# Optimization experiments

Measured on AMD Instinct MI355X. Metric: run time of the kernel, lower is better.

Reference implementation:

```python
import jax, jax.numpy as jnp
import numpy as np

B, S, H = 2, 1024, 2048
E, K, F = 64, 8, 768
CAP = 512


def setup_inputs() -> dict:
    key = jax.random.key(0)
    k1, k2, k3, k4, k5 = jax.random.split(key, 5)
    scale_h = 1.0 / np.sqrt(H)
    scale_f = 1.0 / np.sqrt(F)
    return {
        "hidden_states": jax.random.normal(k1, (B, S, H), jnp.float32),
        "router_w": jax.random.normal(k2, (E, H), jnp.float32) * scale_h,   # MoEGate.weight [E, H]
        "w_gate": jax.random.normal(k3, (E, H, F), jnp.float32) * scale_h,
        "w_up": jax.random.normal(k4, (E, H, F), jnp.float32) * scale_h,
        "w_down": jax.random.normal(k5, (E, F, H), jnp.float32) * scale_f,
    }


def reference(hidden_states, router_w, w_gate, w_up, w_down):
    b, s, h = hidden_states.shape
    T = b * s
    xf = hidden_states.reshape(T, h)

    # --- MoEGate: softmax over expert logits, then top-k, then renormalize ---
    logits = xf @ router_w.T                                   # [T, E]
    scores = jax.nn.softmax(logits.astype(jnp.float32), axis=-1)
    topk_w, topk_idx = jax.lax.top_k(scores, K)                # [T, K]
    topk_w = topk_w / (topk_w.sum(axis=-1, keepdims=True) + 1e-20)

    # --- dispatch: scatter each (token, k) slot into a per-expert capacity buffer ---
    slot_expert = topk_idx.reshape(-1)                         # [T*K]
    slot_token = jnp.repeat(jnp.arange(T), K)                  # [T*K]
    onehot = jax.nn.one_hot(slot_expert, E, dtype=jnp.int32)   # [T*K, E]
    pos = (jnp.cumsum(onehot, axis=0) * onehot).sum(-1) - 1    # position within expert
    valid = pos < CAP
    dest = jnp.where(valid, slot_expert * CAP + pos, E * CAP)  # overflow -> dummy row

    buf = jnp.zeros((E * CAP + 1, h), xf.dtype).at[dest].set(xf[slot_token])
    xb = buf[: E * CAP].reshape(E, CAP, h)                     # [E, CAP, H]

    # --- grouped GEMM experts: SwiGLU MLP per expert ---
    gate = jnp.einsum("ech,ehf->ecf", xb, w_gate)
    up = jnp.einsum("ech,ehf->ecf", xb, w_up)
    hmid = jax.nn.silu(gate) * up                              # [E, CAP, F]
    yb = jnp.einsum("ecf,efh->ech", hmid, w_down).reshape(E * CAP, h)
    yb = jnp.concatenate([yb, jnp.zeros((1, h), yb.dtype)], axis=0)

    # --- combine: gather expert outputs back, weight, scatter-add per token ---
    slot_out = yb[dest] * topk_w.reshape(-1)[:, None].astype(yb.dtype)
    out = jnp.zeros((T, h), yb.dtype).at[slot_token].add(slot_out)
    return out.reshape(b, s, h)
```

## Files before the change

### kernel.cpp

```cpp
#include <hip/hip_runtime.h>
#include <math.h>

#define T_TOK 2048
#define HD    2048
#define NEXP  64
#define KTOP  8
#define FD    768
#define CAPE  512

typedef float  f32x4 __attribute__((ext_vector_type(4)));
typedef __bf16 bf16x8 __attribute__((ext_vector_type(8)));

__device__ __forceinline__ unsigned short f2bf(float f) {
  union { float f; unsigned u; } v; v.f = f;
  unsigned r = v.u + 0x7fffu + ((v.u >> 16) & 1u);
  return (unsigned short)(r >> 16);
}

__device__ __forceinline__ void load_lds16(const void* g, void* l) {
  __builtin_amdgcn_global_load_lds(
      (const __attribute__((address_space(1))) unsigned int*)g,
      (__attribute__((address_space(3))) unsigned int*)l, 16, 0, 0);
}

__global__ __launch_bounds__(256) void router_kernel(
    const float* __restrict__ x, const float* __restrict__ rw,
    int* __restrict__ cnt, int* __restrict__ tok_list, float* __restrict__ w_list)
{
  const int t = threadIdx.x;
  const int tb = blockIdx.x * 4;
  __shared__ float xs[4][HD];
  __shared__ float lg[4][NEXP];

  const float4* xsrc = (const float4*)(x + (size_t)tb * HD);
  float4* xdst = (float4*)&xs[0][0];
  for (int i = t; i < 4 * HD / 4; i += 256) xdst[i] = xsrc[i];
  __syncthreads();

  {
    const int e = t >> 2, q = t & 3;
    const float* wrow = rw + (size_t)e * HD;
    float a0 = 0.f, a1 = 0.f, a2 = 0.f, a3 = 0.f;
    for (int i = 0; i < HD / 16; ++i) {
      int h = (i * 4 + q) * 4;
      float4 wv = *(const float4*)(wrow + h);
      float4 x0 = *(const float4*)&xs[0][h];
      float4 x1 = *(const float4*)&xs[1][h];
      float4 x2 = *(const float4*)&xs[2][h];
      float4 x3 = *(const float4*)&xs[3][h];
      a0 += wv.x*x0.x + wv.y*x0.y + wv.z*x0.z + wv.w*x0.w;
      a1 += wv.x*x1.x + wv.y*x1.y + wv.z*x1.z + wv.w*x1.w;
      a2 += wv.x*x2.x + wv.y*x2.y + wv.z*x2.z + wv.w*x2.w;
      a3 += wv.x*x3.x + wv.y*x3.y + wv.z*x3.z + wv.w*x3.w;
    }
    a0 += __shfl_xor(a0, 1); a0 += __shfl_xor(a0, 2);
    a1 += __shfl_xor(a1, 1); a1 += __shfl_xor(a1, 2);
    a2 += __shfl_xor(a2, 1); a2 += __shfl_xor(a2, 2);
    a3 += __shfl_xor(a3, 1); a3 += __shfl_xor(a3, 2);
    if (q == 0) { lg[0][e] = a0; lg[1][e] = a1; lg[2][e] = a2; lg[3][e] = a3; }
  }
  __syncthreads();

  const int wid = t >> 6, lane = t & 63;
  float v = lg[wid][lane];
  float mx = v;
  for (int o = 32; o; o >>= 1) mx = fmaxf(mx, __shfl_xor(mx, o));
  float p = expf(v - mx);
  float s = p;
  for (int o = 32; o; o >>= 1) s += __shfl_xor(s, o);
  float prob = p / s;

  float r = prob;
  float wk[KTOP]; int ik[KTOP]; float wsum = 0.f;
  #pragma unroll
  for (int k = 0; k < KTOP; ++k) {
    float bv = r; int bl = lane;
    for (int o = 32; o; o >>= 1) {
      float ov = __shfl_xor(bv, o); int ol = __shfl_xor(bl, o);
      if (ov > bv || (ov == bv && ol < bl)) { bv = ov; bl = ol; }
    }
    wk[k] = bv; ik[k] = bl; wsum += bv;
    if (lane == bl) r = -1.f;
  }
  if (lane == 0) {
    float inv = 1.f / (wsum + 1e-20f);
    int token = tb + wid;
    #pragma unroll
    for (int k = 0; k < KTOP; ++k) {
      int ex = ik[k];
      int pos = atomicAdd(&cnt[ex], 1);
      if (pos < CAPE) {
        tok_list[ex * CAPE + pos] = token;
        w_list[ex * CAPE + pos] = wk[k] * inv;
      }
    }
  }
}

__global__ __launch_bounds__(256) void cvt_kernel(
    const float* __restrict__ x, unsigned short* __restrict__ xb)
{
  int i = blockIdx.x * 256 + threadIdx.x;
  float4 v = ((const float4*)x)[i];
  ushort4 o = make_ushort4(f2bf(v.x), f2bf(v.y), f2bf(v.z), f2bf(v.w));
  ((ushort4*)xb)[i] = o;
}

__global__ __launch_bounds__(256) void gateup_kernel(
    const unsigned short* __restrict__ xb,
    const float* __restrict__ wg, const float* __restrict__ wu,
    const int* __restrict__ cnt, const int* __restrict__ tok_list,
    unsigned short* __restrict__ hmid)
{
  const int nt = blockIdx.x, mt = blockIdx.y, e = blockIdx.z;
  int ne = cnt[e]; ne = ne < CAPE ? ne : CAPE;
  if (mt * 128 >= ne) return;
  const int t = threadIdx.x, lane = t & 63, wid = t >> 6;
  const int wr = wid >> 1, wc = wid & 1;

  __shared__ __align__(16) unsigned short A[128 * 64];
  __shared__ __align__(16) unsigned short Bg[64 * 72];
  __shared__ __align__(16) unsigned short Bu[64 * 72];
  __shared__ int toks[128];

  if (t < 128) {
    int r = mt * 128 + t;
    toks[t] = tok_list[e * CAPE + (r < ne ? r : 0)];
  }
  __syncthreads();

  f32x4 z4 = {0.f, 0.f, 0.f, 0.f};
  f32x4 gacc[4][2], uacc[4][2];
  #pragma unroll
  for (int i = 0; i < 4; ++i)
    #pragma unroll
    for (int j = 0; j < 2; ++j) { gacc[i][j] = z4; uacc[i][j] = z4; }

  const size_t wbase = (size_t)e * HD * FD + (size_t)nt * 64;
  const int nc = t & 15, kc = t >> 4;

  for (int kt = 0; kt < HD / 64; ++kt) {
    const int k0 = kt * 64;
    #pragma unroll
    for (int i = 0; i < 4; ++i) {
      const int inst = wid * 4 + i;
      const int G = inst * 64 + lane;
      const int m = G >> 3, gg = G & 7;
      const unsigned short* src = xb + (size_t)toks[m] * HD + k0 + 8 * (gg ^ (m & 7));
      load_lds16(src, &A[inst * 512]);
    }
    {
      const float* pg = wg + wbase + (size_t)(k0 + kc * 4) * FD + nc * 4;
      float4 r0 = *(const float4*)(pg);
      float4 r1 = *(const float4*)(pg + FD);
      float4 r2 = *(const float4*)(pg + 2 * FD);
      float4 r3 = *(const float4*)(pg + 3 * FD);
      *(ushort4*)&Bg[(nc*4+0)*72 + kc*4] = make_ushort4(f2bf(r0.x), f2bf(r1.x), f2bf(r2.x), f2bf(r3.x));
      *(ushort4*)&Bg[(nc*4+1)*72 + kc*4] = make_ushort4(f2bf(r0.y), f2bf(r1.y), f2bf(r2.y), f2bf(r3.y));
      *(ushort4*)&Bg[(nc*4+2)*72 + kc*4] = make_ushort4(f2bf(r0.z), f2bf(r1.z), f2bf(r2.z), f2bf(r3.z));
      *(ushort4*)&Bg[(nc*4+3)*72 + kc*4] = make_ushort4(f2bf(r0.w), f2bf(r1.w), f2bf(r2.w), f2bf(r3.w));
    }
    {
      const float* pu = wu + wbase + (size_t)(k0 + kc * 4) * FD + nc * 4;
      float4 r0 = *(const float4*)(pu);
      float4 r1 = *(const float4*)(pu + FD);
      float4 r2 = *(const float4*)(pu + 2 * FD);
      float4 r3 = *(const float4*)(pu + 3 * FD);
      *(ushort4*)&Bu[(nc*4+0)*72 + kc*4] = make_ushort4(f2bf(r0.x), f2bf(r1.x), f2bf(r2.x), f2bf(r3.x));
      *(ushort4*)&Bu[(nc*4+1)*72 + kc*4] = make_ushort4(f2bf(r0.y), f2bf(r1.y), f2bf(r2.y), f2bf(r3.y));
      *(ushort4*)&Bu[(nc*4+2)*72 + kc*4] = make_ushort4(f2bf(r0.z), f2bf(r1.z), f2bf(r2.z), f2bf(r3.z));
      *(ushort4*)&Bu[(nc*4+3)*72 + kc*4] = make_ushort4(f2bf(r0.w), f2bf(r1.w), f2bf(r2.w), f2bf(r3.w));
    }
    __syncthreads();
    #pragma unroll
    for (int ks = 0; ks < 2; ++ks) {
      bf16x8 af[4];
      #pragma unroll
      for (int mf = 0; mf < 4; ++mf) {
        int row = wr * 64 + mf * 16 + (lane & 15);
        int byte = row * 128 + (lane >> 4) * 16 + ks * 64;
        byte ^= (row & 7) << 4;
        af[mf] = *(const bf16x8*)((const char*)A + byte);
      }
      #pragma unroll
      for (int nf = 0; nf < 2; ++nf) {
        int n = wc * 32 + nf * 16 + (lane & 15);
        int off = n * 72 + (lane >> 4) * 8 + ks * 32;
        bf16x8 bgf = *(const bf16x8*)&Bg[off];
        bf16x8 bum = *(const bf16x8*)&Bu[off];
        #pragma unroll
        for (int mf = 0; mf < 4; ++mf) {
          gacc[mf][nf] = __builtin_amdgcn_mfma_f32_16x16x32_bf16(af[mf], bgf, gacc[mf][nf], 0, 0, 0);
          uacc[mf][nf] = __builtin_amdgcn_mfma_f32_16x16x32_bf16(af[mf], bum, uacc[mf][nf], 0, 0, 0);
        }
      }
    }
    __syncthreads();
  }
  const size_t hbase = (size_t)e * CAPE + (size_t)mt * 128;
  #pragma unroll
  for (int mf = 0; mf < 4; ++mf) {
    #pragma unroll
    for (int nf = 0; nf < 2; ++nf) {
      #pragma unroll
      for (int r = 0; r < 4; ++r) {
        int row = wr * 64 + mf * 16 + (lane >> 4) * 4 + r;
        int c = nt * 64 + wc * 32 + nf * 16 + (lane & 15);
        float gv = gacc[mf][nf][r], uv = uacc[mf][nf][r];
        float hv = gv / (1.f + expf(-gv)) * uv;
        hmid[(hbase + row) * FD + c] = f2bf(hv);
      }
    }
  }
}

__global__ __launch_bounds__(256) void down_kernel(
    const unsigned short* __restrict__ hmid,
    const float* __restrict__ wd,
    const int* __restrict__ cnt, const int* __restrict__ tok_list,
    const float* __restrict__ w_list, float* __restrict__ out)
{
  const int nt = blockIdx.x, mt = blockIdx.y, e = blockIdx.z;
  int ne = cnt[e]; ne = ne < CAPE ? ne : CAPE;
  if (mt * 128 >= ne) return;
  const int t = threadIdx.x, lane = t & 63, wid = t >> 6;
  const int wr = wid >> 1, wc = wid & 1;

  __shared__ __align__(16) unsigned short A[128 * 64];
  __shared__ __align__(16) unsigned short Bd[64 * 72];
  __shared__ int toks[128];
  __shared__ float wts[128];

  if (t < 128) {
    int r = mt * 128 + t;
    bool vv = r < ne;
    toks[t] = vv ? tok_list[e * CAPE + r] : 0;
    wts[t]  = vv ? w_list[e * CAPE + r] : 0.f;
  }

  f32x4 z4 = {0.f, 0.f, 0.f, 0.f};
  f32x4 dacc[4][2];
  #pragma unroll
  for (int i = 0; i < 4; ++i)
    #pragma unroll
    for (int j = 0; j < 2; ++j) dacc[i][j] = z4;

  const size_t wbase = (size_t)e * FD * HD + (size_t)nt * 64;
  const size_t arow = (size_t)e * CAPE + (size_t)mt * 128;
  const int nc = t & 15, kc = t >> 4;

  for (int kt = 0; kt < FD / 64; ++kt) {
    const int k0 = kt * 64;
    #pragma unroll
    for (int i = 0; i < 4; ++i) {
      const int inst = wid * 4 + i;
      const int G = inst * 64 + lane;
      const int m = G >> 3, gg = G & 7;
      const unsigned short* src = hmid + (arow + m) * FD + k0 + 8 * (gg ^ (m & 7));
      load_lds16(src, &A[inst * 512]);
    }
    {
      const float* pd = wd + wbase + (size_t)(k0 + kc * 4) * HD + nc * 4;
      float4 r0 = *(const float4*)(pd);
      float4 r1 = *(const float4*)(pd + HD);
      float4 r2 = *(const float4*)(pd + 2 * HD);
      float4 r3 = *(const float4*)(pd + 3 * HD);
      *(ushort4*)&Bd[(nc*4+0)*72 + kc*4] = make_ushort4(f2bf(r0.x), f2bf(r1.x), f2bf(r2.x), f2bf(r3.x));
      *(ushort4*)&Bd[(nc*4+1)*72 + kc*4] = make_ushort4(f2bf(r0.y), f2bf(r1.y), f2bf(r2.y), f2bf(r3.y));
      *(ushort4*)&Bd[(nc*4+2)*72 + kc*4] = make_ushort4(f2bf(r0.z), f2bf(r1.z), f2bf(r2.z), f2bf(r3.z));
      *(ushort4*)&Bd[(nc*4+3)*72 + kc*4] = make_ushort4(f2bf(r0.w), f2bf(r1.w), f2bf(r2.w), f2bf(r3.w));
    }
    __syncthreads();
    #pragma unroll
    for (int ks = 0; ks < 2; ++ks) {
      bf16x8 af[4];
      #pragma unroll
      for (int mf = 0; mf < 4; ++mf) {
        int row = wr * 64 + mf * 16 + (lane & 15);
        int byte = row * 128 + (lane >> 4) * 16 + ks * 64;
        byte ^= (row & 7) << 4;
        af[mf] = *(const bf16x8*)((const char*)A + byte);
      }
      #pragma unroll
      for (int nf = 0; nf < 2; ++nf) {
        int n = wc * 32 + nf * 16 + (lane & 15);
        int off = n * 72 + (lane >> 4) * 8 + ks * 32;
        bf16x8 bdf = *(const bf16x8*)&Bd[off];
        #pragma unroll
        for (int mf = 0; mf < 4; ++mf)
          dacc[mf][nf] = __builtin_amdgcn_mfma_f32_16x16x32_bf16(af[mf], bdf, dacc[mf][nf], 0, 0, 0);
      }
    }
    __syncthreads();
  }
  #pragma unroll
  for (int mf = 0; mf < 4; ++mf) {
    #pragma unroll
    for (int nf = 0; nf < 2; ++nf) {
      int c = nt * 64 + wc * 32 + nf * 16 + (lane & 15);
      #pragma unroll
      for (int r = 0; r < 4; ++r) {
        int row = wr * 64 + mf * 16 + (lane >> 4) * 4 + r;
        if (mt * 128 + row < ne) {
          int tok = toks[row];
          float w = wts[row];
          atomicAdd(&out[(size_t)tok * HD + c], w * dacc[mf][nf][r]);
        }
      }
    }
  }
}

extern "C" void kernel_launch(void* const* d_in, const int* in_sizes, int n_in,
                              void* d_out, int out_size, void* d_ws, size_t ws_size,
                              hipStream_t stream) {
  const float* x  = (const float*)d_in[0];
  const float* rw = (const float*)d_in[1];
  const float* wg = (const float*)d_in[2];
  const float* wu = (const float*)d_in[3];
  const float* wd = (const float*)d_in[4];
  float* out = (float*)d_out;

  char* ws = (char*)d_ws;
  unsigned short* xb   = (unsigned short*)ws;
  int* cnt             = (int*)(ws + 8388608);
  int* tok_list        = (int*)(ws + 8388864);
  float* w_list        = (float*)(ws + 8519936);
  unsigned short* hmid = (unsigned short*)(ws + 8651008);

  hipMemsetAsync(d_out, 0, (size_t)out_size * sizeof(float), stream);
  hipMemsetAsync(cnt, 0, NEXP * sizeof(int), stream);

  router_kernel<<<T_TOK / 4, 256, 0, stream>>>(x, rw, cnt, tok_list, w_list);
  cvt_kernel<<<(T_TOK * HD / 4) / 256, 256, 0, stream>>>(x, xb);
  gateup_kernel<<<dim3(FD / 64, CAPE / 128, NEXP), 256, 0, stream>>>(xb, wg, wu, cnt, tok_list, hmid);
  down_kernel<<<dim3(HD / 64, CAPE / 128, NEXP), 256, 0, stream>>>(hmid, wd, cnt, tok_list, w_list, out);
}
```

Before: 786.1 us.

## Double-buffer LDS tiles and prefetch weights in gate/up and down GEMMs

Both expert GEMM kernels now double-buffer the A and B shared-memory tiles. The next k-tile's fp32 weights are loaded into registers and its activation rows are issued as async global-to-LDS loads before the MFMA work on the current tile, with the bf16 conversion to LDS happening after the compute, so memory latency overlaps compute and one barrier per iteration is removed. The software f32-to-bf16 rounding is replaced with native __bf16 casts and expf with __expf. In exchange LDS use roughly doubles, which can lower occupancy, and register pressure rises from the prefetch registers.

Result: slower. 846.5 us (+7.7%).

```diff
diff --git a/kernel.cpp b/kernel.cpp
--- a/kernel.cpp
+++ b/kernel.cpp
@@ -10,12 +10,7 @@
 
 typedef float  f32x4 __attribute__((ext_vector_type(4)));
 typedef __bf16 bf16x8 __attribute__((ext_vector_type(8)));
-
-__device__ __forceinline__ unsigned short f2bf(float f) {
-  union { float f; unsigned u; } v; v.f = f;
-  unsigned r = v.u + 0x7fffu + ((v.u >> 16) & 1u);
-  return (unsigned short)(r >> 16);
-}
+typedef __bf16 bf16x4 __attribute__((ext_vector_type(4)));
 
 __device__ __forceinline__ void load_lds16(const void* g, void* l) {
   __builtin_amdgcn_global_load_lds(
@@ -102,8 +97,8 @@
 {
   int i = blockIdx.x * 256 + threadIdx.x;
   float4 v = ((const float4*)x)[i];
-  ushort4 o = make_ushort4(f2bf(v.x), f2bf(v.y), f2bf(v.z), f2bf(v.w));
-  ((ushort4*)xb)[i] = o;
+  bf16x4 o = { (__bf16)v.x, (__bf16)v.y, (__bf16)v.z, (__bf16)v.w };
+  ((bf16x4*)xb)[i] = o;
 }
 
 __global__ __launch_bounds__(256) void gateup_kernel(
@@ -118,9 +113,9 @@
   const int t = threadIdx.x, lane = t & 63, wid = t >> 6;
   const int wr = wid >> 1, wc = wid & 1;
 
-  __shared__ __align__(16) unsigned short A[128 * 64];
-  __shared__ __align__(16) unsigned short Bg[64 * 72];
-  __shared__ __align__(16) unsigned short Bu[64 * 72];
+  __shared__ __align__(16) unsigned short A[2 * 128 * 64];
+  __shared__ __align__(16) unsigned short Bg[2 * 64 * 72];
+  __shared__ __align__(16) unsigned short Bu[2 * 64 * 72];
   __shared__ int toks[128];
 
   if (t < 128) {
@@ -138,40 +133,53 @@
 
   const size_t wbase = (size_t)e * HD * FD + (size_t)nt * 64;
   const int nc = t & 15, kc = t >> 4;
+  float4 rg0, rg1, rg2, rg3, ru0, ru1, ru2, ru3;
+
+#define LOAD_B_GU(K0) do { \
+    const float* pg = wg + wbase + (size_t)((K0) + kc * 4) * FD + nc * 4; \
+    const float* pu = wu + wbase + (size_t)((K0) + kc * 4) * FD + nc * 4; \
+    rg0 = *(const float4*)pg;          rg1 = *(const float4*)(pg + FD); \
+    rg2 = *(const float4*)(pg + 2*FD); rg3 = *(const float4*)(pg + 3*FD); \
+    ru0 = *(const float4*)pu;          ru1 = *(const float4*)(pu + FD); \
+    ru2 = *(const float4*)(pu + 2*FD); ru3 = *(const float4*)(pu + 3*FD); \
+  } while (0)
+
+#define STAGE_A_GU(KT, BUF) do { \
+    const int k0s = (KT) * 64; \
+    _Pragma("unroll") \
+    for (int i_ = 0; i_ < 4; ++i_) { \
+      const int inst = wid * 4 + i_; \
+      const int G = inst * 64 + lane; \
+      const int m = G >> 3, gg = G & 7; \
+      load_lds16(xb + (size_t)toks[m] * HD + k0s + 8 * (gg ^ (m & 7)), \
+                 &A[(BUF) * 8192 + inst * 512]); \
+    } \
+  } while (0)
+
+#define CVT_B(DST, BUF, r0, r1, r2, r3) do { \
+    __bf16* bb = (__bf16*)&(DST)[(BUF) * 4608]; \
+    *(bf16x4*)&bb[(nc*4+0)*72 + kc*4] = (bf16x4){(__bf16)r0.x,(__bf16)r1.x,(__bf16)r2.x,(__bf16)r3.x}; \
+    *(bf16x4*)&bb[(nc*4+1)*72 + kc*4] = (bf16x4){(__bf16)r0.y,(__bf16)r1.y,(__bf16)r2.y,(__bf16)r3.y}; \
+    *(bf16x4*)&bb[(nc*4+2)*72 + kc*4] = (bf16x4){(__bf16)r0.z,(__bf16)r1.z,(__bf16)r2.z,(__bf16)r3.z}; \
+    *(bf16x4*)&bb[(nc*4+3)*72 + kc*4] = (bf16x4){(__bf16)r0.w,(__bf16)r1.w,(__bf16)r2.w,(__bf16)r3.w}; \
+  } while (0)
+
+  LOAD_B_GU(0);
+  STAGE_A_GU(0, 0);
+  CVT_B(Bg, 0, rg0, rg1, rg2, rg3);
+  CVT_B(Bu, 0, ru0, ru1, ru2, ru3);
+  __syncthreads();
 
   for (int kt = 0; kt < HD / 64; ++kt) {
-    const int k0 = kt * 64;
-    #pragma unroll
-    for (int i = 0; i < 4; ++i) {
-      const int inst = wid * 4 + i;
-      const int G = inst * 64 + lane;
-      const int m = G >> 3, gg = G & 7;
-      const unsigned short* src = xb + (size_t)toks[m] * HD + k0 + 8 * (gg ^ (m & 7));
-      load_lds16(src, &A[inst * 512]);
-    }
-    {
-      const float* pg = wg + wbase + (size_t)(k0 + kc * 4) * FD + nc * 4;
-      float4 r0 = *(const float4*)(pg);
-      float4 r1 = *(const float4*)(pg + FD);
-      float4 r2 = *(const float4*)(pg + 2 * FD);
-      float4 r3 = *(const float4*)(pg + 3 * FD);
-      *(ushort4*)&Bg[(nc*4+0)*72 + kc*4] = make_ushort4(f2bf(r0.x), f2bf(r1.x), f2bf(r2.x), f2bf(r3.x));
-      *(ushort4*)&Bg[(nc*4+1)*72 + kc*4] = make_ushort4(f2bf(r0.y), f2bf(r1.y), f2bf(r2.y), f2bf(r3.y));
-      *(ushort4*)&Bg[(nc*4+2)*72 + kc*4] = make_ushort4(f2bf(r0.z), f2bf(r1.z), f2bf(r2.z), f2bf(r3.z));
-      *(ushort4*)&Bg[(nc*4+3)*72 + kc*4] = make_ushort4(f2bf(r0.w), f2bf(r1.w), f2bf(r2.w), f2bf(r3.w));
-    }
-    {
-      const float* pu = wu + wbase + (size_t)(k0 + kc * 4) * FD + nc * 4;
-      float4 r0 = *(const float4*)(pu);
-      float4 r1 = *(const float4*)(pu + FD);
-      float4 r2 = *(const float4*)(pu + 2 * FD);
-      float4 r3 = *(const float4*)(pu + 3 * FD);
-      *(ushort4*)&Bu[(nc*4+0)*72 + kc*4] = make_ushort4(f2bf(r0.x), f2bf(r1.x), f2bf(r2.x), f2bf(r3.x));
-      *(ushort4*)&Bu[(nc*4+1)*72 + kc*4] = make_ushort4(f2bf(r0.y), f2bf(r1.y), f2bf(r2.y), f2bf(r3.y));
-      *(ushort4*)&Bu[(nc*4+2)*72 + kc*4] = make_ushort4(f2bf(r0.z), f2bf(r1.z), f2bf(r2.z), f2bf(r3.z));
-      *(ushort4*)&Bu[(nc*4+3)*72 + kc*4] = make_ushort4(f2bf(r0.w), f2bf(r1.w), f2bf(r2.w), f2bf(r3.w));
-    }
-    __syncthreads();
+    const int cur = kt & 1;
+    const bool more = (kt + 1) < HD / 64;
+    if (more) {
+      LOAD_B_GU((kt + 1) * 64);
+      STAGE_A_GU(kt + 1, cur ^ 1);
+    }
+    const char* Ab = (const char*)&A[cur * 8192];
+    const unsigned short* BgB = &Bg[cur * 4608];
+    const unsigned short* BuB = &Bu[cur * 4608];
     #pragma unroll
     for (int ks = 0; ks < 2; ++ks) {
       bf16x8 af[4];
@@ -180,14 +188,14 @@
         int row = wr * 64 + mf * 16 + (lane & 15);
         int byte = row * 128 + (lane >> 4) * 16 + ks * 64;
         byte ^= (row & 7) << 4;
-        af[mf] = *(const bf16x8*)((const char*)A + byte);
+        af[mf] = *(const bf16x8*)(Ab + byte);
       }
       #pragma unroll
       for (int nf = 0; nf < 2; ++nf) {
         int n = wc * 32 + nf * 16 + (lane & 15);
         int off = n * 72 + (lane >> 4) * 8 + ks * 32;
-        bf16x8 bgf = *(const bf16x8*)&Bg[off];
-        bf16x8 bum = *(const bf16x8*)&Bu[off];
+        bf16x8 bgf = *(const bf16x8*)&BgB[off];
+        bf16x8 bum = *(const bf16x8*)&BuB[off];
         #pragma unroll
         for (int mf = 0; mf < 4; ++mf) {
           gacc[mf][nf] = __builtin_amdgcn_mfma_f32_16x16x32_bf16(af[mf], bgf, gacc[mf][nf], 0, 0, 0);
@@ -195,9 +203,17 @@
         }
       }
     }
+    if (more) {
+      CVT_B(Bg, cur ^ 1, rg0, rg1, rg2, rg3);
+      CVT_B(Bu, cur ^ 1, ru0, ru1, ru2, ru3);
+    }
     __syncthreads();
   }
+#undef LOAD_B_GU
+#undef STAGE_A_GU
+
   const size_t hbase = (size_t)e * CAPE + (size_t)mt * 128;
+  __bf16* hm = (__bf16*)hmid;
   #pragma unroll
   for (int mf = 0; mf < 4; ++mf) {
     #pragma unroll
@@ -207,8 +223,8 @@
         int row = wr * 64 + mf * 16 + (lane >> 4) * 4 + r;
         int c = nt * 64 + wc * 32 + nf * 16 + (lane & 15);
         float gv = gacc[mf][nf][r], uv = uacc[mf][nf][r];
-        float hv = gv / (1.f + expf(-gv)) * uv;
-        hmid[(hbase + row) * FD + c] = f2bf(hv);
+        float hv = gv / (1.f + __expf(-gv)) * uv;
+        hm[(hbase + row) * FD + c] = (__bf16)hv;
       }
     }
   }
@@ -226,8 +242,8 @@
   const int t = threadIdx.x, lane = t & 63, wid = t >> 6;
   const int wr = wid >> 1, wc = wid & 1;
 
-  __shared__ __align__(16) unsigned short A[128 * 64];
-  __shared__ __align__(16) unsigned short Bd[64 * 72];
+  __shared__ __align__(16) unsigned short A[2 * 128 * 64];
+  __shared__ __align__(16) unsigned short Bd[2 * 64 * 72];
   __shared__ int toks[128];
   __shared__ float wts[128];
 
@@ -237,6 +253,7 @@
     toks[t] = vv ? tok_list[e * CAPE + r] : 0;
     wts[t]  = vv ? w_list[e * CAPE + r] : 0.f;
   }
+  __syncthreads();
 
   f32x4 z4 = {0.f, 0.f, 0.f, 0.f};
   f32x4 dacc[4][2];
@@ -248,29 +265,40 @@
   const size_t wbase = (size_t)e * FD * HD + (size_t)nt * 64;
   const size_t arow = (size_t)e * CAPE + (size_t)mt * 128;
   const int nc = t & 15, kc = t >> 4;
+  float4 rd0, rd1, rd2, rd3;
+
+#define LOAD_B_D(K0) do { \
+    const float* pd = wd + wbase + (size_t)((K0) + kc * 4) * HD + nc * 4; \
+    rd0 = *(const float4*)pd;          rd1 = *(const float4*)(pd + HD); \
+    rd2 = *(const float4*)(pd + 2*HD); rd3 = *(const float4*)(pd + 3*HD); \
+  } while (0)
+
+#define STAGE_A_D(KT, BUF) do { \
+    const int k0s = (KT) * 64; \
+    _Pragma("unroll") \
+    for (int i_ = 0; i_ < 4; ++i_) { \
+      const int inst = wid * 4 + i_; \
+      const int G = inst * 64 + lane; \
+      const int m = G >> 3, gg = G & 7; \
+      load_lds16(hmid + (arow + m) * FD + k0s + 8 * (gg ^ (m & 7)), \
+                 &A[(BUF) * 8192 + inst * 512]); \
+    } \
+  } while (0)
+
+  LOAD_B_D(0);
+  STAGE_A_D(0, 0);
+  CVT_B(Bd, 0, rd0, rd1, rd2, rd3);
+  __syncthreads();
 
   for (int kt = 0; kt < FD / 64; ++kt) {
-    const int k0 = kt * 64;
-    #pragma unroll
-    for (int i = 0; i < 4; ++i) {
-      const int inst = wid * 4 + i;
-      const int G = inst * 64 + lane;
-      const int m = G >> 3, gg = G & 7;
-      const unsigned short* src = hmid + (arow + m) * FD + k0 + 8 * (gg ^ (m & 7));
-      load_lds16(src, &A[inst * 512]);
-    }
-    {
-      const float* pd = wd + wbase + (size_t)(k0 + kc * 4) * HD + nc * 4;
-      float4 r0 = *(const float4*)(pd);
-      float4 r1 = *(const float4*)(pd + HD);
-      float4 r2 = *(const float4*)(pd + 2 * HD);
-      float4 r3 = *(const float4*)(pd + 3 * HD);
-      *(ushort4*)&Bd[(nc*4+0)*72 + kc*4] = make_ushort4(f2bf(r0.x), f2bf(r1.x), f2bf(r2.x), f2bf(r3.x));
-      *(ushort4*)&Bd[(nc*4+1)*72 + kc*4] = make_ushort4(f2bf(r0.y), f2bf(r1.y), f2bf(r2.y), f2bf(r3.y));
-      *(ushort4*)&Bd[(nc*4+2)*72 + kc*4] = make_ushort4(f2bf(r0.z), f2bf(r1.z), f2bf(r2.z), f2bf(r3.z));
-      *(ushort4*)&Bd[(nc*4+3)*72 + kc*4] = make_ushort4(f2bf(r0.w), f2bf(r1.w), f2bf(r2.w), f2bf(r3.w));
-    }
-    __syncthreads();
+    const int cur = kt & 1;
+    const bool more = (kt + 1) < FD / 64;
+    if (more) {
+      LOAD_B_D((kt + 1) * 64);
+      STAGE_A_D(kt + 1, cur ^ 1);
+    }
+    const char* Ab = (const char*)&A[cur * 8192];
+    const unsigned short* BdB = &Bd[cur * 4608];
     #pragma unroll
     for (int ks = 0; ks < 2; ++ks) {
       bf16x8 af[4];
@@ -279,20 +307,25 @@
         int row = wr * 64 + mf * 16 + (lane & 15);
         int byte = row * 128 + (lane >> 4) * 16 + ks * 64;
         byte ^= (row & 7) << 4;
-        af[mf] = *(const bf16x8*)((const char*)A + byte);
+        af[mf] = *(const bf16x8*)(Ab + byte);
       }
       #pragma unroll
       for (int nf = 0; nf < 2; ++nf) {
         int n = wc * 32 + nf * 16 + (lane & 15);
         int off = n * 72 + (lane >> 4) * 8 + ks * 32;
-        bf16x8 bdf = *(const bf16x8*)&Bd[off];
+        bf16x8 bdf = *(const bf16x8*)&BdB[off];
         #pragma unroll
         for (int mf = 0; mf < 4; ++mf)
           dacc[mf][nf] = __builtin_amdgcn_mfma_f32_16x16x32_bf16(af[mf], bdf, dacc[mf][nf], 0, 0, 0);
       }
     }
+    if (more) CVT_B(Bd, cur ^ 1, rd0, rd1, rd2, rd3);
     __syncthreads();
   }
+#undef LOAD_B_D
+#undef STAGE_A_D
+#undef CVT_B
+
   #pragma unroll
   for (int mf = 0; mf < 4; ++mf) {
     #pragma unroll
```

## Double-buffer LDS and software-pipeline weight loads in gate/up and down GEMMs

Applied to the files above, without the earlier changes.

Both expert GEMM kernels move to double-buffered LDS tiles with register-prefetched fp32 weight loads and manual vmcnt/lgkmcnt waits, so global loads for the next K tile overlap MFMA work on the current one. B tiles in LDS gain an XOR swizzle, and conversions use native bf16 casts plus a fast exp. Launch bounds request two blocks per CU. The hand-counted waitcnt values are fragile: if the compiler reorders or splits the loads, reads could race. The larger LDS footprint may also limit occupancy.

Result: faster. 654.2 us (-16.8%).

```diff
diff --git a/kernel.cpp b/kernel.cpp
--- a/kernel.cpp
+++ b/kernel.cpp
@@ -10,18 +10,16 @@
 
 typedef float  f32x4 __attribute__((ext_vector_type(4)));
 typedef __bf16 bf16x8 __attribute__((ext_vector_type(8)));
-
-__device__ __forceinline__ unsigned short f2bf(float f) {
-  union { float f; unsigned u; } v; v.f = f;
-  unsigned r = v.u + 0x7fffu + ((v.u >> 16) & 1u);
-  return (unsigned short)(r >> 16);
-}
+typedef __bf16 bf16x4 __attribute__((ext_vector_type(4)));
 
 __device__ __forceinline__ void load_lds16(const void* g, void* l) {
   __builtin_amdgcn_global_load_lds(
       (const __attribute__((address_space(1))) unsigned int*)g,
       (__attribute__((address_space(3))) unsigned int*)l, 16, 0, 0);
 }
+
+#define WAITCNT(S) asm volatile(S ::: "memory")
+#define BARRIER()  __builtin_amdgcn_s_barrier()
 
 __global__ __launch_bounds__(256) void router_kernel(
     const float* __restrict__ x, const float* __restrict__ rw,
@@ -101,12 +99,13 @@
     const float* __restrict__ x, unsigned short* __restrict__ xb)
 {
   int i = blockIdx.x * 256 + threadIdx.x;
-  float4 v = ((const float4*)x)[i];
-  ushort4 o = make_ushort4(f2bf(v.x), f2bf(v.y), f2bf(v.z), f2bf(v.w));
-  ((ushort4*)xb)[i] = o;
-}
-
-__global__ __launch_bounds__(256) void gateup_kernel(
+  f32x4 v = ((const f32x4*)x)[i];
+  bf16x4 o = { (__bf16)v[0], (__bf16)v[1], (__bf16)v[2], (__bf16)v[3] };
+  ((bf16x4*)xb)[i] = o;
+}
+
+
+__global__ __launch_bounds__(256, 2) void gateup_kernel(
     const unsigned short* __restrict__ xb,
     const float* __restrict__ wg, const float* __restrict__ wu,
     const int* __restrict__ cnt, const int* __restrict__ tok_list,
@@ -118,9 +117,9 @@
   const int t = threadIdx.x, lane = t & 63, wid = t >> 6;
   const int wr = wid >> 1, wc = wid & 1;
 
-  __shared__ __align__(16) unsigned short A[128 * 64];
-  __shared__ __align__(16) unsigned short Bg[64 * 72];
-  __shared__ __align__(16) unsigned short Bu[64 * 72];
+  __shared__ __align__(16) unsigned short A[2 * 128 * 64];
+  __shared__ __align__(16) unsigned short Bg[2 * 64 * 72];
+  __shared__ __align__(16) unsigned short Bu[2 * 64 * 72];
   __shared__ int toks[128];
 
   if (t < 128) {
@@ -129,6 +128,15 @@
   }
   __syncthreads();
 
+  const unsigned short* asrc[4];
+  #pragma unroll
+  for (int i = 0; i < 4; ++i) {
+    const int inst = wid * 4 + i;
+    const int G = inst * 64 + lane;
+    const int m = G >> 3, gg = G & 7;
+    asrc[i] = xb + (size_t)toks[m] * HD + 8 * (gg ^ (m & 7));
+  }
+
   f32x4 z4 = {0.f, 0.f, 0.f, 0.f};
   f32x4 gacc[4][2], uacc[4][2];
   #pragma unroll
@@ -138,66 +146,105 @@
 
   const size_t wbase = (size_t)e * HD * FD + (size_t)nt * 64;
   const int nc = t & 15, kc = t >> 4;
-
-  for (int kt = 0; kt < HD / 64; ++kt) {
-    const int k0 = kt * 64;
-    #pragma unroll
-    for (int i = 0; i < 4; ++i) {
-      const int inst = wid * 4 + i;
-      const int G = inst * 64 + lane;
-      const int m = G >> 3, gg = G & 7;
-      const unsigned short* src = xb + (size_t)toks[m] * HD + k0 + 8 * (gg ^ (m & 7));
-      load_lds16(src, &A[inst * 512]);
-    }
-    {
-      const float* pg = wg + wbase + (size_t)(k0 + kc * 4) * FD + nc * 4;
-      float4 r0 = *(const float4*)(pg);
-      float4 r1 = *(const float4*)(pg + FD);
-      float4 r2 = *(const float4*)(pg + 2 * FD);
-      float4 r3 = *(const float4*)(pg + 3 * FD);
-      *(ushort4*)&Bg[(nc*4+0)*72 + kc*4] = make_ushort4(f2bf(r0.x), f2bf(r1.x), f2bf(r2.x), f2bf(r3.x));
-      *(ushort4*)&Bg[(nc*4+1)*72 + kc*4] = make_ushort4(f2bf(r0.y), f2bf(r1.y), f2bf(r2.y), f2bf(r3.y));
-      *(ushort4*)&Bg[(nc*4+2)*72 + kc*4] = make_ushort4(f2bf(r0.z), f2bf(r1.z), f2bf(r2.z), f2bf(r3.z));
-      *(ushort4*)&Bg[(nc*4+3)*72 + kc*4] = make_ushort4(f2bf(r0.w), f2bf(r1.w), f2bf(r2.w), f2bf(r3.w));
-    }
-    {
-      const float* pu = wu + wbase + (size_t)(k0 + kc * 4) * FD + nc * 4;
-      float4 r0 = *(const float4*)(pu);
-      float4 r1 = *(const float4*)(pu + FD);
-      float4 r2 = *(const float4*)(pu + 2 * FD);
-      float4 r3 = *(const float4*)(pu + 3 * FD);
-      *(ushort4*)&Bu[(nc*4+0)*72 + kc*4] = make_ushort4(f2bf(r0.x), f2bf(r1.x), f2bf(r2.x), f2bf(r3.x));
-      *(ushort4*)&Bu[(nc*4+1)*72 + kc*4] = make_ushort4(f2bf(r0.y), f2bf(r1.y), f2bf(r2.y), f2bf(r3.y));
-      *(ushort4*)&Bu[(nc*4+2)*72 + kc*4] = make_ushort4(f2bf(r0.z), f2bf(r1.z), f2bf(r2.z), f2bf(r3.z));
-      *(ushort4*)&Bu[(nc*4+3)*72 + kc*4] = make_ushort4(f2bf(r0.w), f2bf(r1.w), f2bf(r2.w), f2bf(r3.w));
-    }
-    __syncthreads();
-    #pragma unroll
-    for (int ks = 0; ks < 2; ++ks) {
-      bf16x8 af[4];
-      #pragma unroll
-      for (int mf = 0; mf < 4; ++mf) {
-        int row = wr * 64 + mf * 16 + (lane & 15);
-        int byte = row * 128 + (lane >> 4) * 16 + ks * 64;
-        byte ^= (row & 7) << 4;
-        af[mf] = *(const bf16x8*)((const char*)A + byte);
-      }
-      #pragma unroll
-      for (int nf = 0; nf < 2; ++nf) {
-        int n = wc * 32 + nf * 16 + (lane & 15);
-        int off = n * 72 + (lane >> 4) * 8 + ks * 32;
-        bf16x8 bgf = *(const bf16x8*)&Bg[off];
-        bf16x8 bum = *(const bf16x8*)&Bu[off];
-        #pragma unroll
-        for (int mf = 0; mf < 4; ++mf) {
-          gacc[mf][nf] = __builtin_amdgcn_mfma_f32_16x16x32_bf16(af[mf], bgf, gacc[mf][nf], 0, 0, 0);
-          uacc[mf][nf] = __builtin_amdgcn_mfma_f32_16x16x32_bf16(af[mf], bum, uacc[mf][nf], 0, 0, 0);
-        }
-      }
-    }
-    __syncthreads();
-  }
+  f32x4 Ra[8], Rb[8];
+
+#define LOAD_GU(K0, R) do { \
+    const float* pg_ = wg + wbase + (size_t)((K0) + kc * 4) * FD + nc * 4; \
+    const float* pu_ = wu + wbase + (size_t)((K0) + kc * 4) * FD + nc * 4; \
+    R[0] = *(const f32x4*)pg_;            R[1] = *(const f32x4*)(pg_ + FD); \
+    R[2] = *(const f32x4*)(pg_ + 2*FD);   R[3] = *(const f32x4*)(pg_ + 3*FD); \
+    R[4] = *(const f32x4*)pu_;            R[5] = *(const f32x4*)(pu_ + FD); \
+    R[6] = *(const f32x4*)(pu_ + 2*FD);   R[7] = *(const f32x4*)(pu_ + 3*FD); \
+  } while (0)
+
+#define STAGE_A4(KT, BUF) do { \
+    const int k0s_ = (KT) * 64; \
+    _Pragma("unroll") \
+    for (int i_ = 0; i_ < 4; ++i_) \
+      load_lds16(asrc[i_] + k0s_, &A[(BUF) * 8192 + (wid * 4 + i_) * 512]); \
+  } while (0)
+
+#define CVT_GU(BUF, R) do { \
+    __bf16* bg_ = (__bf16*)&Bg[(BUF) * 4608]; \
+    __bf16* bu_ = (__bf16*)&Bu[(BUF) * 4608]; \
+    const int xm_ = (nc & 7) << 3; \
+    _Pragma("unroll") \
+    for (int j_ = 0; j_ < 4; ++j_) { \
+      int so_ = (nc * 4 + j_) * 72 + ((kc * 4) ^ xm_); \
+      *(bf16x4*)&bg_[so_] = (bf16x4){(__bf16)R[0][j_], (__bf16)R[1][j_], (__bf16)R[2][j_], (__bf16)R[3][j_]}; \
+      *(bf16x4*)&bu_[so_] = (bf16x4){(__bf16)R[4][j_], (__bf16)R[5][j_], (__bf16)R[6][j_], (__bf16)R[7][j_]}; \
+    } \
+  } while (0)
+
+#define COMPUTE_GU(CUR) do { \
+    const char* Ab_ = (const char*)&A[(CUR) * 8192]; \
+    const __bf16* Bg_ = (const __bf16*)&Bg[(CUR) * 4608]; \
+    const __bf16* Bu_ = (const __bf16*)&Bu[(CUR) * 4608]; \
+    _Pragma("unroll") \
+    for (int ks = 0; ks < 2; ++ks) { \
+      bf16x8 af[4]; \
+      _Pragma("unroll") \
+      for (int mf = 0; mf < 4; ++mf) { \
+        int row = wr * 64 + mf * 16 + (lane & 15); \
+        int byte = row * 128 + (lane >> 4) * 16 + ks * 64; \
+        byte ^= (row & 7) << 4; \
+        af[mf] = *(const bf16x8*)(Ab_ + byte); \
+      } \
+      _Pragma("unroll") \
+      for (int nf = 0; nf < 2; ++nf) { \
+        int n = wc * 32 + nf * 16 + (lane & 15); \
+        int so = n * 72 + ((((lane >> 4) * 8) + ks * 32) ^ (((n >> 2) & 7) << 3)); \
+        bf16x8 bgf = *(const bf16x8*)&Bg_[so]; \
+        bf16x8 bum = *(const bf16x8*)&Bu_[so]; \
+        _Pragma("unroll") \
+        for (int mf = 0; mf < 4; ++mf) { \
+          gacc[mf][nf] = __builtin_amdgcn_mfma_f32_16x16x32_bf16(af[mf], bgf, gacc[mf][nf], 0, 0, 0); \
+          uacc[mf][nf] = __builtin_amdgcn_mfma_f32_16x16x32_bf16(af[mf], bum, uacc[mf][nf], 0, 0, 0); \
+        } \
+      } \
+    } \
+  } while (0)
+
+  LOAD_GU(0, Ra);
+  STAGE_A4(0, 0);
+  LOAD_GU(64, Rb);
+  WAITCNT("s_waitcnt vmcnt(12)");
+  CVT_GU(0, Ra);
+  WAITCNT("s_waitcnt vmcnt(8) lgkmcnt(0)");
+  BARRIER();
+
+  for (int i = 0; i < 15; ++i) {
+    const int kt = 2 * i;
+    STAGE_A4(kt + 1, 1);
+    LOAD_GU((kt + 2) * 64, Ra);
+    WAITCNT("s_waitcnt vmcnt(12)");
+    CVT_GU(1, Rb);
+    COMPUTE_GU(0);
+    WAITCNT("s_waitcnt vmcnt(8) lgkmcnt(0)");
+    BARRIER();
+
+    STAGE_A4(kt + 2, 0);
+    LOAD_GU((kt + 3) * 64, Rb);
+    WAITCNT("s_waitcnt vmcnt(12)");
+    CVT_GU(0, Ra);
+    COMPUTE_GU(1);
+    WAITCNT("s_waitcnt vmcnt(8) lgkmcnt(0)");
+    BARRIER();
+  }
+  STAGE_A4(31, 1);
+  CVT_GU(1, Rb);
+  COMPUTE_GU(0);
+  WAITCNT("s_waitcnt vmcnt(0) lgkmcnt(0)");
+  BARRIER();
+  COMPUTE_GU(1);
+
+#undef LOAD_GU
+#undef STAGE_A4
+#undef CVT_GU
+#undef COMPUTE_GU
+
   const size_t hbase = (size_t)e * CAPE + (size_t)mt * 128;
+  __bf16* hm = (__bf16*)hmid;
   #pragma unroll
   for (int mf = 0; mf < 4; ++mf) {
     #pragma unroll
@@ -207,14 +254,14 @@
         int row = wr * 64 + mf * 16 + (lane >> 4) * 4 + r;
         int c = nt * 64 + wc * 32 + nf * 16 + (lane & 15);
         float gv = gacc[mf][nf][r], uv = uacc[mf][nf][r];
-        float hv = gv / (1.f + expf(-gv)) * uv;
-        hmid[(hbase + row) * FD + c] = f2bf(hv);
+        float hv = gv / (1.f + __expf(-gv)) * uv;
+        hm[(hbase + row) * FD + c] = (__bf16)hv;
       }
     }
   }
 }
 
-__global__ __launch_bounds__(256) void down_kernel(
+__global__ __launch_bounds__(256, 2) void down_kernel(
     const unsigned short* __restrict__ hmid,
     const float* __restrict__ wd,
     const int* __restrict__ cnt, const int* __restrict__ tok_list,
@@ -226,8 +273,8 @@
   const int t = threadIdx.x, lane = t & 63, wid = t >> 6;
   const int wr = wid >> 1, wc = wid & 1;
 
-  __shared__ __align__(16) unsigned short A[128 * 64];
-  __shared__ __align__(16) unsigned short Bd[64 * 72];
+  __shared__ __align__(16) unsigned short A[2 * 128 * 64];
+  __shared__ __align__(16) unsigned short Bd[2 * 64 * 72];
   __shared__ int toks[128];
   __shared__ float wts[128];
 
@@ -237,6 +284,17 @@
     toks[t] = vv ? tok_list[e * CAPE + r] : 0;
     wts[t]  = vv ? w_list[e * CAPE + r] : 0.f;
   }
+  __syncthreads();
+
+  const size_t arow = (size_t)e * CAPE + (size_t)mt * 128;
+  const unsigned short* asrc[4];
+  #pragma unroll
+  for (int i = 0; i < 4; ++i) {
+    const int inst = wid * 4 + i;
+    const int G = inst * 64 + lane;
+    const int m = G >> 3, gg = G & 7;
+    asrc[i] = hmid + (arow + m) * FD + 8 * (gg ^ (m & 7));
+  }
 
   f32x4 z4 = {0.f, 0.f, 0.f, 0.f};
   f32x4 dacc[4][2];
@@ -246,53 +304,95 @@
     for (int j = 0; j < 2; ++j) dacc[i][j] = z4;
 
   const size_t wbase = (size_t)e * FD * HD + (size_t)nt * 64;
-  const size_t arow = (size_t)e * CAPE + (size_t)mt * 128;
   const int nc = t & 15, kc = t >> 4;
-
-  for (int kt = 0; kt < FD / 64; ++kt) {
-    const int k0 = kt * 64;
-    #pragma unroll
-    for (int i = 0; i < 4; ++i) {
-      const int inst = wid * 4 + i;
-      const int G = inst * 64 + lane;
-      const int m = G >> 3, gg = G & 7;
-      const unsigned short* src = hmid + (arow + m) * FD + k0 + 8 * (gg ^ (m & 7));
-      load_lds16(src, &A[inst * 512]);
-    }
-    {
-      const float* pd = wd + wbase + (size_t)(k0 + kc * 4) * HD + nc * 4;
-      float4 r0 = *(const float4*)(pd);
-      float4 r1 = *(const float4*)(pd + HD);
-      float4 r2 = *(const float4*)(pd + 2 * HD);
-      float4 r3 = *(const float4*)(pd + 3 * HD);
-      *(ushort4*)&Bd[(nc*4+0)*72 + kc*4] = make_ushort4(f2bf(r0.x), f2bf(r1.x), f2bf(r2.x), f2bf(r3.x));
-      *(ushort4*)&Bd[(nc*4+1)*72 + kc*4] = make_ushort4(f2bf(r0.y), f2bf(r1.y), f2bf(r2.y), f2bf(r3.y));
-      *(ushort4*)&Bd[(nc*4+2)*72 + kc*4] = make_ushort4(f2bf(r0.z), f2bf(r1.z), f2bf(r2.z), f2bf(r3.z));
-      *(ushort4*)&Bd[(nc*4+3)*72 + kc*4] = make_ushort4(f2bf(r0.w), f2bf(r1.w), f2bf(r2.w), f2bf(r3.w));
-    }
-    __syncthreads();
-    #pragma unroll
-    for (int ks = 0; ks < 2; ++ks) {
-      bf16x8 af[4];
-      #pragma unroll
-      for (int mf = 0; mf < 4; ++mf) {
-        int row = wr * 64 + mf * 16 + (lane & 15);
-        int byte = row * 128 + (lane >> 4) * 16 + ks * 64;
-        byte ^= (row & 7) << 4;
-        af[mf] = *(const bf16x8*)((const char*)A + byte);
-      }
-      #pragma unroll
-      for (int nf = 0; nf < 2; ++nf) {
-        int n = wc * 32 + nf * 16 + (lane & 15);
-        int off = n * 72 + (lane >> 4) * 8 + ks * 32;
-        bf16x8 bdf = *(const bf16x8*)&Bd[off];
-        #pragma unroll
-        for (int mf = 0; mf < 4; ++mf)
-          dacc[mf][nf] = __builtin_amdgcn_mfma_f32_16x16x32_bf16(af[mf], bdf, dacc[mf][nf], 0, 0, 0);
-      }
-    }
-    __syncthreads();
-  }
+  f32x4 Ra[4], Rb[4];
+
+#define LOAD_D(K0, R) do { \
+    const float* pd_ = wd + wbase + (size_t)((K0) + kc * 4) * HD + nc * 4; \
+    R[0] = *(const f32x4*)pd_;            R[1] = *(const f32x4*)(pd_ + HD); \
+    R[2] = *(const f32x4*)(pd_ + 2*HD);   R[3] = *(const f32x4*)(pd_ + 3*HD); \
+  } while (0)
+
+#define STAGE_A4(KT, BUF) do { \
+    const int k0s_ = (KT) * 64; \
+    _Pragma("unroll") \
+    for (int i_ = 0; i_ < 4; ++i_) \
+      load_lds16(asrc[i_] + k0s_, &A[(BUF) * 8192 + (wid * 4 + i_) * 512]); \
+  } while (0)
+
+#define CVT_D(BUF, R) do { \
+    __bf16* bd_ = (__bf16*)&Bd[(BUF) * 4608]; \
+    const int xm_ = (nc & 7) << 3; \
+    _Pragma("unroll") \
+    for (int j_ = 0; j_ < 4; ++j_) { \
+      int so_ = (nc * 4 + j_) * 72 + ((kc * 4) ^ xm_); \
+      *(bf16x4*)&bd_[so_] = (bf16x4){(__bf16)R[0][j_], (__bf16)R[1][j_], (__bf16)R[2][j_], (__bf16)R[3][j_]}; \
+    } \
+  } while (0)
+
+#define COMPUTE_D(CUR) do { \
+    const char* Ab_ = (const char*)&A[(CUR) * 8192]; \
+    const __bf16* Bd_ = (const __bf16*)&Bd[(CUR) * 4608]; \
+    _Pragma("unroll") \
+    for (int ks = 0; ks < 2; ++ks) { \
+      bf16x8 af[4]; \
+      _Pragma("unroll") \
+      for (int mf = 0; mf < 4; ++mf) { \
+        int row = wr * 64 + mf * 16 + (lane & 15); \
+        int byte = row * 128 + (lane >> 4) * 16 + ks * 64; \
+        byte ^= (row & 7) << 4; \
+        af[mf] = *(const bf16x8*)(Ab_ + byte); \
+      } \
+      _Pragma("unroll") \
+      for (int nf = 0; nf < 2; ++nf) { \
+        int n = wc * 32 + nf * 16 + (lane & 15); \
+        int so = n * 72 + ((((lane >> 4) * 8) + ks * 32) ^ (((n >> 2) & 7) << 3)); \
+        bf16x8 bdf = *(const bf16x8*)&Bd_[so]; \
+        _Pragma("unroll") \
+        for (int mf = 0; mf < 4; ++mf) \
+          dacc[mf][nf] = __builtin_amdgcn_mfma_f32_16x16x32_bf16(af[mf], bdf, dacc[mf][nf], 0, 0, 0); \
+      } \
+    } \
+  } while (0)
+
+  LOAD_D(0, Ra);
+  STAGE_A4(0, 0);
+  LOAD_D(64, Rb);
+  WAITCNT("s_waitcnt vmcnt(8)");
+  CVT_D(0, Ra);
+  WAITCNT("s_waitcnt vmcnt(4) lgkmcnt(0)");
+  BARRIER();
+
+  for (int i = 0; i < 5; ++i) {
+    const int kt = 2 * i;
+    STAGE_A4(kt + 1, 1);
+    LOAD_D((kt + 2) * 64, Ra);
+    WAITCNT("s_waitcnt vmcnt(8)");
+    CVT_D(1, Rb);
+    COMPUTE_D(0);
+    WAITCNT("s_waitcnt vmcnt(4) lgkmcnt(0)");
+    BARRIER();
+
+    STAGE_A4(kt + 2, 0);
+    LOAD_D((kt + 3) * 64, Rb);
+    WAITCNT("s_waitcnt vmcnt(8)");
+    CVT_D(0, Ra);
+    COMPUTE_D(1);
+    WAITCNT("s_waitcnt vmcnt(4) lgkmcnt(0)");
+    BARRIER();
+  }
+  STAGE_A4(11, 1);
+  CVT_D(1, Rb);
+  COMPUTE_D(0);
+  WAITCNT("s_waitcnt vmcnt(0) lgkmcnt(0)");
+  BARRIER();
+  COMPUTE_D(1);
+
+#undef LOAD_D
+#undef STAGE_A4
+#undef CVT_D
+#undef COMPUTE_D
+
   #pragma unroll
   for (int mf = 0; mf < 4; ++mf) {
     #pragma unroll
```
